# Optimization experiments

Measured on AMD Instinct MI355X. Metric: run time of the kernel, lower is better.

The kernel has to match this reference:

```python
import jax, jax.numpy as jnp
import numpy as np

N, E, G = 50000, 800000, 512
DIN, HID, DOUT, L, DE = 64, 64, 128, 3, 16
NEG_SLOPE = 0.2
BN_EPS = 1e-5


def setup_inputs() -> dict:
    key = jax.random.key(0)
    ks = jax.random.split(key, 20)
    s = 0.1  # weight scale for numerical stability
    return {
        "x": jax.random.normal(ks[0], (N, DIN), jnp.float32),
        "edge_index": jax.random.randint(ks[1], (2, E), 0, N, jnp.int32),
        "edge_attr": jax.random.normal(ks[2], (E, DE), jnp.float32),
        "batch": jnp.sort(jax.random.randint(ks[3], (N,), 0, G, jnp.int32)),
        "emb_W": jax.random.normal(ks[4], (HID, DIN), jnp.float32) * s,
        "emb_b": jax.random.normal(ks[5], (HID,), jnp.float32) * s,
        "Wl": jax.random.normal(ks[6], (L, HID, HID), jnp.float32) * s,
        "bl": jax.random.normal(ks[7], (L, HID), jnp.float32) * s,
        "Wr": jax.random.normal(ks[8], (L, HID, HID), jnp.float32) * s,
        "br": jax.random.normal(ks[9], (L, HID), jnp.float32) * s,
        "We": jax.random.normal(ks[10], (L, HID, DE), jnp.float32) * s,
        "att": jax.random.normal(ks[11], (L, HID), jnp.float32) * s,
        "conv_bias": jax.random.normal(ks[12], (L, HID), jnp.float32) * s,
        "bn_gamma": jax.random.uniform(ks[13], (L, HID), jnp.float32, 0.5, 1.5),
        "bn_beta": jax.random.normal(ks[14], (L, HID), jnp.float32) * s,
        "bn_mean": jnp.zeros((L, HID), jnp.float32),
        "bn_var": jnp.ones((L, HID), jnp.float32),
        "lin_W": jax.random.normal(ks[15], (DOUT, HID), jnp.float32) * s,
        "lin_b": jax.random.normal(ks[16], (DOUT,), jnp.float32) * s,
    }


def _gatv2(h, src, dst, edge_attr, Wl, bl, Wr, br, We, att, bias):
    # GATv2Conv, heads=1, concat=False, with edge features
    xl = h @ Wl.T + bl                      # [N,C] source transform (also message value)
    xr = h @ Wr.T + br                      # [N,C] target transform
    ea = edge_attr @ We.T                   # [E,C]
    m = xl[src] + xr[dst] + ea              # [E,C]
    m = jax.nn.leaky_relu(m, NEG_SLOPE)
    alpha = m @ att                         # [E] attention logits
    amax = jax.ops.segment_max(alpha, dst, num_segments=N)
    ea_exp = jnp.exp(alpha - amax[dst])
    denom = jax.ops.segment_sum(ea_exp, dst, num_segments=N)
    alpha = ea_exp / (denom[dst] + 1e-16)
    out = jax.ops.segment_sum(alpha[:, None] * xl[src], dst, num_segments=N)
    return out + bias


def reference(x, edge_index, edge_attr, batch, emb_W, emb_b, Wl, bl, Wr, br,
              We, att, conv_bias, bn_gamma, bn_beta, bn_mean, bn_var, lin_W, lin_b):
    src, dst = edge_index[0], edge_index[1]
    h = x @ emb_W.T + emb_b
    for i in range(L):
        hc = _gatv2(h, src, dst, edge_attr, Wl[i], bl[i], Wr[i], br[i],
                    We[i], att[i], conv_bias[i])
        # BatchNorm (eval mode, running stats)
        hc = (hc - bn_mean[i]) * jax.lax.rsqrt(bn_var[i] + BN_EPS) * bn_gamma[i] + bn_beta[i]
        hc = jax.nn.gelu(hc, approximate=False)  # torch F.gelu default is exact erf
        h = h + hc                                # residual; dropout p=0 / eval -> identity
    out = h @ lin_W.T + lin_b                     # [N,DOUT]
    counts = jax.ops.segment_sum(jnp.ones((N,), out.dtype), batch, num_segments=G)
    pooled = jax.ops.segment_sum(out, batch, num_segments=G)
    return pooled / jnp.maximum(counts, 1.0)[:, None]
```

## Files before the change

kernel.cpp:

```cpp
#include <hip/hip_runtime.h>
#include <math.h>

#define NEG_SLOPE 0.2f
#define BN_EPS 1e-5f

template <int N> struct IC { static constexpr int v = N; };
template <bool B> struct BC { static constexpr bool v = B; };

typedef _Float16 half2v __attribute__((ext_vector_type(2)));

__device__ __forceinline__ half2v u2h(unsigned u) {
  union { unsigned u; half2v h; } c;
  c.u = u;
  return c.h;
}
__device__ __forceinline__ unsigned pkh(float lo, float hi) {
  union { half2v h; unsigned u; } c;
  c.h[0] = (_Float16)lo;
  c.h[1] = (_Float16)hi;
  return c.u;
}

#if defined(__has_builtin)
#if __has_builtin(__builtin_amdgcn_fdot2)
#define FDOT2(a, b, c) __builtin_amdgcn_fdot2((a), (b), (c), false)
#endif
#endif
#ifndef FDOT2
__device__ __forceinline__ float fdot2_sw(half2v a, half2v b, float c) {
  return c + (float)a[0] * (float)b[0] + (float)a[1] * (float)b[1];
}
#define FDOT2(a, b, c) fdot2_sw((a), (b), (c))
#endif

#if defined(__has_builtin)
#if __has_builtin(__builtin_amdgcn_exp2f)
#define FEXP(x) __builtin_amdgcn_exp2f(x)
#define ATT_SCALE 1.44269504088896f
#endif
#endif
#ifndef FEXP
#define FEXP(x) __expf(x)
#define ATT_SCALE 1.0f
#endif

#define FMA4(acc, v, wq) \
  acc += (v).x * (wq).x + (v).y * (wq).y + (v).z * (wq).z + (v).w * (wq).w

#define DOT_ROW(buf, r, bias, OUT)                                     \
  {                                                                    \
    __builtin_amdgcn_sched_barrier(0);                                 \
    float a0 = 0.f, a1 = 0.f, a2 = 0.f, a3 = 0.f;                      \
    _Pragma("unroll") for (int q = 0; q < 4; q++) {                    \
      float4 v0 = *(const float4*)((buf) + (r) * 64 + q * 16 + 0);     \
      float4 v1 = *(const float4*)((buf) + (r) * 64 + q * 16 + 4);     \
      float4 v2 = *(const float4*)((buf) + (r) * 64 + q * 16 + 8);     \
      float4 v3 = *(const float4*)((buf) + (r) * 64 + q * 16 + 12);    \
      FMA4(a0, v0, W[q * 4 + 0]);                                      \
      FMA4(a1, v1, W[q * 4 + 1]);                                      \
      FMA4(a2, v2, W[q * 4 + 2]);                                      \
      FMA4(a3, v3, W[q * 4 + 3]);                                      \
    }                                                                  \
    OUT = (bias) + ((a0 + a1) + (a2 + a3));                            \
  }

__device__ __forceinline__ float wave_sum64(float v) {
  int x;
  x = __builtin_amdgcn_update_dpp(0, __float_as_int(v), 0x121, 0xF, 0xF, true);
  v += __int_as_float(x);
  x = __builtin_amdgcn_update_dpp(0, __float_as_int(v), 0x122, 0xF, 0xF, true);
  v += __int_as_float(x);
  x = __builtin_amdgcn_update_dpp(0, __float_as_int(v), 0x124, 0xF, 0xF, true);
  v += __int_as_float(x);
  x = __builtin_amdgcn_update_dpp(0, __float_as_int(v), 0x128, 0xF, 0xF, true);
  v += __int_as_float(x);
  x = __builtin_amdgcn_update_dpp(0, __float_as_int(v), 0x142, 0xF, 0xF, true);
  v += __int_as_float(x);
  x = __builtin_amdgcn_update_dpp(0, __float_as_int(v), 0x143, 0xF, 0xF, true);
  v += __int_as_float(x);
  return __int_as_float(__builtin_amdgcn_readlane(__float_as_int(v), 63));
}

__global__ __launch_bounds__(256) void hist_kernel(
    const int* __restrict__ dst, const int* __restrict__ batch,
    int* __restrict__ deg, float* __restrict__ counts, int E_, int N_) {
  int i = blockIdx.x * 256 + threadIdx.x;
  if (i < E_) atomicAdd(&deg[dst[i]], 1);
  if (i < N_) atomicAdd(&counts[batch[i]], 1.0f);
}

__global__ __launch_bounds__(256) void scanA_kernel(
    const int* __restrict__ deg, int* __restrict__ row_ptr,
    int* __restrict__ segTot, int N_, int nseg) {
  __shared__ int sb[256];
  int t = threadIdx.x;
  for (int s = blockIdx.x; s < nseg; s += gridDim.x) {
    int i = s * 256 + t;
    int v = (i < N_) ? deg[i] : 0;
    sb[t] = v;
    __syncthreads();
    for (int off = 1; off < 256; off <<= 1) {
      int a = (t >= off) ? sb[t - off] : 0;
      __syncthreads();
      sb[t] += a;
      __syncthreads();
    }
    int incl = sb[t];
    if (i < N_) row_ptr[i] = incl - v;
    if (t == 255) segTot[s] = incl;
    __syncthreads();
  }
}

__global__ __launch_bounds__(256) void scanB_kernel(int* __restrict__ segTot,
                                                    int nseg) {
  __shared__ int sb[256];
  __shared__ int baseSh;
  int t = threadIdx.x;
  if (t == 0) baseSh = 0;
  __syncthreads();
  for (int c0 = 0; c0 < nseg; c0 += 256) {
    int s = c0 + t;
    int v = (s < nseg) ? segTot[s] : 0;
    sb[t] = v;
    __syncthreads();
    for (int off = 1; off < 256; off <<= 1) {
      int a = (t >= off) ? sb[t - off] : 0;
      __syncthreads();
      sb[t] += a;
      __syncthreads();
    }
    int incl = sb[t];
    int base = baseSh;
    if (s < nseg) segTot[s] = base + incl - v;
    __syncthreads();
    if (t == 255) baseSh = base + incl;
    __syncthreads();
  }
}

__global__ __launch_bounds__(256) void scanC_kernel(
    int* __restrict__ row_ptr, const int* __restrict__ segTot,
    int* __restrict__ cursor, int N_, int E_) {
  int tid = blockIdx.x * 256 + threadIdx.x;
  int nt = gridDim.x * 256;
  for (int i = tid; i < N_; i += nt) {
    int rp = row_ptr[i] + segTot[i >> 8];
    row_ptr[i] = rp;
    cursor[i] = rp;
  }
  if (tid == 0) row_ptr[N_] = E_;
}

__global__ __launch_bounds__(256) void scatter_kernel(
    const int* __restrict__ src, const int* __restrict__ dst,
    int* __restrict__ cursor, int* __restrict__ csr_src,
    int* __restrict__ csr_eid, int E_) {
  int e = blockIdx.x * 256 + threadIdx.x;
  if (e >= E_) return;
  int pos = atomicAdd(&cursor[dst[e]], 1);
  csr_src[pos] = src[e];
  csr_eid[pos] = e;
}

__global__ __launch_bounds__(256) void permute_attr_kernel(
    const float4* __restrict__ edge_attr4, const int* __restrict__ csr_eid,
    unsigned* __restrict__ attr_u, int E_) {
  int p = blockIdx.x * 256 + threadIdx.x;
  if (p >= E_) return;
  int e = csr_eid[p];
  float4 a0 = edge_attr4[(size_t)e * 4 + 0];
  float4 a1 = edge_attr4[(size_t)e * 4 + 1];
  float4 a2 = edge_attr4[(size_t)e * 4 + 2];
  float4 a3 = edge_attr4[(size_t)e * 4 + 3];
  uint4 u0, u1;
  u0.x = pkh(a0.x, a0.y);
  u0.y = pkh(a0.z, a0.w);
  u0.z = pkh(a1.x, a1.y);
  u0.w = pkh(a1.z, a1.w);
  u1.x = pkh(a2.x, a2.y);
  u1.y = pkh(a2.z, a2.w);
  u1.z = pkh(a3.x, a3.y);
  u1.w = pkh(a3.z, a3.w);
  uint4* d4 = (uint4*)(attr_u + (size_t)p * 8);
  d4[0] = u0;
  d4[1] = u1;
}

__global__ __launch_bounds__(256, 3) void emb_lin0_kernel(
    const float* __restrict__ x, const float* __restrict__ emb_W,
    const float* __restrict__ emb_b, const float* __restrict__ Wl0,
    const float* __restrict__ bl0, const float* __restrict__ Wr0,
    const float* __restrict__ br0, float* __restrict__ h,
    _Float16* __restrict__ xl, _Float16* __restrict__ xr, int rows) {
  __shared__ float sx[4096];
  __shared__ float sh[4096];
  int lane = threadIdx.x & 63;
  int w = threadIdx.x >> 6;
  int n0 = blockIdx.x * 64;

  {
    int gmax = rows * 64 - 4;
#pragma unroll
    for (int i = 0; i < 4; i++) {
      int off = w * 1024 + i * 256 + lane * 4;
      int g = min(n0 * 64 + off, gmax);
      *(float4*)(sx + off) = *(const float4*)(x + g);
    }
  }

  float4 W[16];
  float b;

#pragma unroll
  for (int q = 0; q < 16; q++) W[q] = ((const float4*)(emb_W + lane * 64))[q];
  b = emb_b[lane];
#pragma unroll 1
  for (int t = 0; t < 16; t++) {
    int r = w * 16 + t;
    float a;
    DOT_ROW(sx, r, b, a);
    sh[r * 64 + lane] = a;
    int n = n0 + r;
    if (n < rows) h[(size_t)n * 64 + lane] = a;
  }

#pragma unroll
  for (int q = 0; q < 16; q++) W[q] = ((const float4*)(Wl0 + lane * 64))[q];
  b = bl0[lane];
#pragma unroll 1
  for (int t = 0; t < 16; t++) {
    int r = w * 16 + t;
    float a;
    DOT_ROW(sh, r, b, a);
    int n = n0 + r;
    if (n < rows) xl[(size_t)n * 64 + lane] = (_Float16)a;
  }

#pragma unroll
  for (int q = 0; q < 16; q++) W[q] = ((const float4*)(Wr0 + lane * 64))[q];
  b = br0[lane];
#pragma unroll 1
  for (int t = 0; t < 16; t++) {
    int r = w * 16 + t;
    float a;
    DOT_ROW(sh, r, b, a);
    int n = n0 + r;
    if (n < rows) xr[(size_t)n * 64 + lane] = (_Float16)a;
  }
}

__global__ __launch_bounds__(256, 3) void linx2_kernel(
    const float* __restrict__ in, const float* __restrict__ Wl,
    const float* __restrict__ bl, const float* __restrict__ Wr,
    const float* __restrict__ br, _Float16* __restrict__ xl,
    _Float16* __restrict__ xr, int rows) {
  __shared__ float sx[4096];
  int lane = threadIdx.x & 63;
  int w = threadIdx.x >> 6;
  int n0 = blockIdx.x * 64;

  {
    int gmax = rows * 64 - 4;
#pragma unroll
    for (int i = 0; i < 4; i++) {
      int off = w * 1024 + i * 256 + lane * 4;
      int g = min(n0 * 64 + off, gmax);
      *(float4*)(sx + off) = *(const float4*)(in + g);
    }
  }

  float4 W[16];
  float b;

#pragma unroll
  for (int q = 0; q < 16; q++) W[q] = ((const float4*)(Wl + lane * 64))[q];
  b = bl[lane];
#pragma unroll 1
  for (int t = 0; t < 16; t++) {
    int r = w * 16 + t;
    float a;
    DOT_ROW(sx, r, b, a);
    int n = n0 + r;
    if (n < rows) xl[(size_t)n * 64 + lane] = (_Float16)a;
  }

#pragma unroll
  for (int q = 0; q < 16; q++) W[q] = ((const float4*)(Wr + lane * 64))[q];
  b = br[lane];
#pragma unroll 1
  for (int t = 0; t < 16; t++) {
    int r = w * 16 + t;
    float a;
    DOT_ROW(sx, r, b, a);
    int n = n0 + r;
    if (n < rows) xr[(size_t)n * 64 + lane] = (_Float16)a;
  }
}

template <bool CONTIG>
__global__ __launch_bounds__(256) void gat_fused_kernel(
    const int* __restrict__ csr_src, const int* __restrict__ csr_eid,
    const int* __restrict__ row_ptr, const unsigned* __restrict__ attr_u,
    const float* __restrict__ edge_attr, const _Float16* __restrict__ xl,
    const _Float16* __restrict__ xr, const float* __restrict__ We,
    const float* __restrict__ att, const float* __restrict__ conv_bias,
    const float* __restrict__ gamma, const float* __restrict__ beta,
    const float* __restrict__ mean, const float* __restrict__ var,
    float* __restrict__ h, int N_) {
  int d = (blockIdx.x * 256 + threadIdx.x) >> 6;
  if (d >= N_) return;
  int j = threadIdx.x & 63;
  half2v Wek2[8];
  float Wekf[16];
  if constexpr (CONTIG) {
#pragma unroll
    for (int q = 0; q < 8; q++) {
      Wek2[q][0] = (_Float16)We[j * 16 + 2 * q];
      Wek2[q][1] = (_Float16)We[j * 16 + 2 * q + 1];
    }
  } else {
#pragma unroll
    for (int k = 0; k < 16; k++) Wekf[k] = We[j * 16 + k];
  }
  float att_j = att[j] * ATT_SCALE;
  float sc = rsqrtf(var[j] + BN_EPS) * gamma[j];
  float sh = (conv_bias[j] - mean[j]) * sc + beta[j];

  int beg = __builtin_amdgcn_readfirstlane(row_ptr[d]);
  int end = __builtin_amdgcn_readfirstlane(row_ptr[d + 1]);
  float xrj = (float)xr[(size_t)d * 64 + j];
  float m = -INFINITY, l = 0.f, acc = 0.f;

  auto chunk = [&](int base, auto C_, auto PAD_) {
    constexpr int C = decltype(C_)::v;
    constexpr bool PAD = decltype(PAD_)::v;
    int si[C];
#pragma unroll
    for (int t = 0; t < C; t++) {
      int idx = PAD ? min(base + t, end - 1) : (base + t);
      si[t] = csr_src[idx];
    }
    float xlv[C];
#pragma unroll
    for (int t = 0; t < C; t++)
      xlv[t] = (float)xl[(size_t)si[t] * 64 + j];
    float v[C];
#pragma unroll
    for (int t = 0; t < C; t++) {
      int idx = PAD ? min(base + t, end - 1) : (base + t);
      float ea;
      if constexpr (CONTIG) {
        const uint4* ap = (const uint4*)(attr_u + (size_t)idx * 8);
        uint4 ua = ap[0], ub = ap[1];
        ea = 0.f;
        ea = FDOT2(u2h(ua.x), Wek2[0], ea);
        ea = FDOT2(u2h(ua.y), Wek2[1], ea);
        ea = FDOT2(u2h(ua.z), Wek2[2], ea);
        ea = FDOT2(u2h(ua.w), Wek2[3], ea);
        ea = FDOT2(u2h(ub.x), Wek2[4], ea);
        ea = FDOT2(u2h(ub.y), Wek2[5], ea);
        ea = FDOT2(u2h(ub.z), Wek2[6], ea);
        ea = FDOT2(u2h(ub.w), Wek2[7], ea);
      } else {
        const float4* ap =
            (const float4*)(edge_attr + (size_t)csr_eid[idx] * 16);
        float4 a0 = ap[0], a1 = ap[1], a2 = ap[2], a3 = ap[3];
        ea = a0.x * Wekf[0]  + a0.y * Wekf[1]  + a0.z * Wekf[2]  + a0.w * Wekf[3]
           + a1.x * Wekf[4]  + a1.y * Wekf[5]  + a1.z * Wekf[6]  + a1.w * Wekf[7]
           + a2.x * Wekf[8]  + a2.y * Wekf[9]  + a2.z * Wekf[10] + a2.w * Wekf[11]
           + a3.x * Wekf[12] + a3.y * Wekf[13] + a3.z * Wekf[14] + a3.w * Wekf[15];
      }
      float z = xlv[t] + xrj + ea;
      z = fmaxf(z, NEG_SLOPE * z);
      float p = wave_sum64(z * att_j);
      v[t] = (!PAD || (base + t < end)) ? p : -INFINITY;
    }
    float mc = v[0];
#pragma unroll
    for (int t = 1; t < C; t++) mc = fmaxf(mc, v[t]);
    float newm = fmaxf(m, mc);
    float s = FEXP(m - newm);
    l *= s;
    acc *= s;
#pragma unroll
    for (int t = 0; t < C; t++) {
      float w = FEXP(v[t] - newm);
      l += w;
      acc += w * xlv[t];
    }
    m = newm;
  };

  int base = beg;
  for (; base + 16 <= end; base += 16) chunk(base, IC<16>{}, BC<false>{});
  if (base + 8 <= end) {
    chunk(base, IC<8>{}, BC<false>{});
    base += 8;
  }
  if (base < end) chunk(base, IC<8>{}, BC<true>{});

  float val = acc / (l + 1e-16f) * sc + sh;
  float g = 0.5f * val * (1.f + erff(val * 0.70710678118654752f));
  h[(size_t)d * 64 + j] += g;
}

__global__ __launch_bounds__(256, 2) void lin_pool_kernel(
    const float* __restrict__ h, const float* __restrict__ lin_W,
    const float* __restrict__ lin_b, const int* __restrict__ batch,
    const float* __restrict__ counts, float* __restrict__ pooled, int rows) {
  __shared__ float shh[4096];
  int lane = threadIdx.x & 63;
  int w = threadIdx.x >> 6;
  int n0 = blockIdx.x * 64;

  {
    int gmax = rows * 64 - 4;
#pragma unroll
    for (int i = 0; i < 4; i++) {
      int off = w * 1024 + i * 256 + lane * 4;
      int g = min(n0 * 64 + off, gmax);
      *(float4*)(shh + off) = *(const float4*)(h + g);
    }
  }

  float4 W0[16], W1[16];
#pragma unroll
  for (int q = 0; q < 16; q++) W0[q] = ((const float4*)(lin_W + lane * 64))[q];
#pragma unroll
  for (int q = 0; q < 16; q++)
    W1[q] = ((const float4*)(lin_W + (lane + 64) * 64))[q];
  float b0 = lin_b[lane], b1 = lin_b[lane + 64];

  int curg = -1;
  float acc0 = 0.f, acc1 = 0.f;
  int lim = min(16, rows - n0 - w * 16);
#pragma unroll 1
  for (int t = 0; t < lim; t++) {
    int r = w * 16 + t;
    __builtin_amdgcn_sched_barrier(0);
    float d0 = b0, d1 = b1;
#pragma unroll
    for (int q = 0; q < 16; q++) {
      float4 v = *(const float4*)(shh + r * 64 + q * 4);
      FMA4(d0, v, W0[q]);
      FMA4(d1, v, W1[q]);
    }
    int g = batch[n0 + r];
    if (g != curg) {
      if (curg >= 0) {
        float inv = 1.f / fmaxf(counts[curg], 1.f);
        atomicAdd(&pooled[curg * 128 + lane], acc0 * inv);
        atomicAdd(&pooled[curg * 128 + 64 + lane], acc1 * inv);
      }
      curg = g;
      acc0 = 0.f;
      acc1 = 0.f;
    }
    acc0 += d0;
    acc1 += d1;
  }
  if (curg >= 0) {
    float inv = 1.f / fmaxf(counts[curg], 1.f);
    atomicAdd(&pooled[curg * 128 + lane], acc0 * inv);
    atomicAdd(&pooled[curg * 128 + 64 + lane], acc1 * inv);
  }
}

extern "C" void kernel_launch(void* const* d_in, const int* in_sizes, int n_in,
                              void* d_out, int out_size, void* d_ws, size_t ws_size,
                              hipStream_t stream) {
  const float* x         = (const float*)d_in[0];
  const int*   edge_index= (const int*)  d_in[1];
  const float* edge_attr = (const float*)d_in[2];
  const int*   batch     = (const int*)  d_in[3];
  const float* emb_W     = (const float*)d_in[4];
  const float* emb_b     = (const float*)d_in[5];
  const float* Wl        = (const float*)d_in[6];
  const float* bl        = (const float*)d_in[7];
  const float* Wr        = (const float*)d_in[8];
  const float* br        = (const float*)d_in[9];
  const float* We        = (const float*)d_in[10];
  const float* att       = (const float*)d_in[11];
  const float* conv_bias = (const float*)d_in[12];
  const float* bn_gamma  = (const float*)d_in[13];
  const float* bn_beta   = (const float*)d_in[14];
  const float* bn_mean   = (const float*)d_in[15];
  const float* bn_var    = (const float*)d_in[16];
  const float* lin_W     = (const float*)d_in[17];
  const float* lin_b     = (const float*)d_in[18];

  const int N_ = in_sizes[0] / 64;
  const int E_ = in_sizes[1] / 2;
  const int G_ = out_size / 128;
  const int* src = edge_index;
  const int* dst = edge_index + E_;

  const int Npad = (N_ + 3) & ~3;
  const int Epad = (E_ + 19) & ~3;
  const int nseg = (N_ + 255) / 256;

  float* ws      = (float*)d_ws;
  float* h       = ws;
  _Float16* xl   = (_Float16*)(h + (size_t)N_ * 64);
  _Float16* xr   = xl + (size_t)N_ * 64;
  int*   csr_src = (int*)(xr + (size_t)N_ * 64);
  int*   csr_eid = csr_src + Epad;
  int*   row_ptr = csr_eid + Epad;
  int*   cursor  = row_ptr + (Npad + 4);
  int*   deg     = cursor + Npad;
  float* counts  = (float*)(deg + Npad);
  int*   segTot  = (int*)(counts + G_);
  uintptr_t abp  = (uintptr_t)(segTot + nseg + 8);
  abp = (abp + 15) & ~(uintptr_t)15;
  unsigned* attr_u = (unsigned*)abp;

  size_t base_bytes = (abp - (uintptr_t)d_ws);
  bool contig = ws_size >= base_bytes + (size_t)E_ * 32 + 64;

  const int hgrid = (max(E_, N_) + 255) / 256;
  const int ngrid = (N_ + 255) / 256;
  const int egrid = (E_ + 255) / 256;

  hipMemsetAsync(deg, 0, ((size_t)Npad + G_) * 4, stream);
  hist_kernel<<<hgrid, 256, 0, stream>>>(dst, batch, deg, counts, E_, N_);
  scanA_kernel<<<min(nseg, 1024), 256, 0, stream>>>(deg, row_ptr, segTot, N_,
                                                    nseg);
  scanB_kernel<<<1, 256, 0, stream>>>(segTot, nseg);
  scanC_kernel<<<ngrid, 256, 0, stream>>>(row_ptr, segTot, cursor, N_, E_);
  scatter_kernel<<<egrid, 256, 0, stream>>>(src, dst, cursor, csr_src,
                                            csr_eid, E_);
  if (contig) {
    permute_attr_kernel<<<egrid, 256, 0, stream>>>(
        (const float4*)edge_attr, csr_eid, attr_u, E_);
  }

  const int tgrid = (N_ + 63) / 64;
  emb_lin0_kernel<<<tgrid, 256, 0, stream>>>(x, emb_W, emb_b, Wl, bl, Wr, br,
                                             h, xl, xr, N_);

  const int gatBlocks = (N_ + 3) / 4;
  for (int l = 0; l < 3; l++) {
    if (l > 0) {
      linx2_kernel<<<tgrid, 256, 0, stream>>>(
          h, Wl + (size_t)l * 4096, bl + l * 64, Wr + (size_t)l * 4096,
          br + l * 64, xl, xr, N_);
    }
    if (contig) {
      gat_fused_kernel<true><<<gatBlocks, 256, 0, stream>>>(
          csr_src, csr_eid, row_ptr, attr_u, edge_attr, xl, xr,
          We + (size_t)l * 1024, att + l * 64, conv_bias + l * 64,
          bn_gamma + l * 64, bn_beta + l * 64, bn_mean + l * 64,
          bn_var + l * 64, h, N_);
    } else {
      gat_fused_kernel<false><<<gatBlocks, 256, 0, stream>>>(
          csr_src, csr_eid, row_ptr, attr_u, edge_attr, xl, xr,
          We + (size_t)l * 1024, att + l * 64, conv_bias + l * 64,
          bn_gamma + l * 64, bn_beta + l * 64, bn_mean + l * 64,
          bn_var + l * 64, h, N_);
    }
  }

  hipMemsetAsync(d_out, 0, (size_t)G_ * 128 * 4, stream);
  lin_pool_kernel<<<(N_ + 63) / 64, 256, 0, stream>>>(
      h, lin_W, lin_b, batch, counts, (float*)d_out, N_);
}
```

Baseline: 627.7 us.

## Map one node row per thread with weights read as uniform loads

```diff
diff --git a/kernel.cpp b/kernel.cpp
--- a/kernel.cpp
+++ b/kernel.cpp
@@ -47,21 +47,21 @@
 #define FMA4(acc, v, wq) \
   acc += (v).x * (wq).x + (v).y * (wq).y + (v).z * (wq).z + (v).w * (wq).w
 
-#define DOT_ROW(buf, r, bias, OUT)                                     \
-  {                                                                    \
-    __builtin_amdgcn_sched_barrier(0);                                 \
-    float a0 = 0.f, a1 = 0.f, a2 = 0.f, a3 = 0.f;                      \
-    _Pragma("unroll") for (int q = 0; q < 4; q++) {                    \
-      float4 v0 = *(const float4*)((buf) + (r) * 64 + q * 16 + 0);     \
-      float4 v1 = *(const float4*)((buf) + (r) * 64 + q * 16 + 4);     \
-      float4 v2 = *(const float4*)((buf) + (r) * 64 + q * 16 + 8);     \
-      float4 v3 = *(const float4*)((buf) + (r) * 64 + q * 16 + 12);    \
-      FMA4(a0, v0, W[q * 4 + 0]);                                      \
-      FMA4(a1, v1, W[q * 4 + 1]);                                      \
-      FMA4(a2, v2, W[q * 4 + 2]);                                      \
-      FMA4(a3, v3, W[q * 4 + 3]);                                      \
-    }                                                                  \
-    OUT = (bias) + ((a0 + a1) + (a2 + a3));                            \
+#define WDOT(Wp, bias, OUT)                                   \
+  {                                                           \
+    __builtin_amdgcn_sched_barrier(0);                        \
+    float a0 = 0.f, a1 = 0.f, a2 = 0.f, a3 = 0.f;             \
+    _Pragma("unroll") for (int k = 0; k < 4; k++) {           \
+      float4 w0 = ((const float4*)(Wp))[k * 4 + 0];           \
+      float4 w1 = ((const float4*)(Wp))[k * 4 + 1];           \
+      float4 w2 = ((const float4*)(Wp))[k * 4 + 2];           \
+      float4 w3 = ((const float4*)(Wp))[k * 4 + 3];           \
+      FMA4(a0, R[k * 4 + 0], w0);                             \
+      FMA4(a1, R[k * 4 + 1], w1);                             \
+      FMA4(a2, R[k * 4 + 2], w2);                             \
+      FMA4(a3, R[k * 4 + 3], w3);                             \
+    }                                                         \
+    OUT = (bias) + ((a0 + a1) + (a2 + a3));                   \
   }
 
 __device__ __forceinline__ float wave_sum64(float v) {
@@ -187,114 +187,77 @@
   d4[1] = u1;
 }
 
-__global__ __launch_bounds__(256, 3) void emb_lin0_kernel(
+__global__ __launch_bounds__(64) void emb_kernel(
     const float* __restrict__ x, const float* __restrict__ emb_W,
-    const float* __restrict__ emb_b, const float* __restrict__ Wl0,
-    const float* __restrict__ bl0, const float* __restrict__ Wr0,
-    const float* __restrict__ br0, float* __restrict__ h,
-    _Float16* __restrict__ xl, _Float16* __restrict__ xr, int rows) {
-  __shared__ float sx[4096];
-  __shared__ float sh[4096];
+    const float* __restrict__ emb_b, float* __restrict__ h, int rows) {
   int lane = threadIdx.x & 63;
-  int w = threadIdx.x >> 6;
-  int n0 = blockIdx.x * 64;
-
+  int n = blockIdx.x * 64 + lane;
+  int nc = min(n, rows - 1);
+  float4 R[16];
   {
-    int gmax = rows * 64 - 4;
-#pragma unroll
-    for (int i = 0; i < 4; i++) {
-      int off = w * 1024 + i * 256 + lane * 4;
-      int g = min(n0 * 64 + off, gmax);
-      *(float4*)(sx + off) = *(const float4*)(x + g);
-    }
-  }
-
-  float4 W[16];
-  float b;
-
-#pragma unroll
-  for (int q = 0; q < 16; q++) W[q] = ((const float4*)(emb_W + lane * 64))[q];
-  b = emb_b[lane];
+    const float4* xp = (const float4*)(x + (size_t)nc * 64);
+#pragma unroll
+    for (int q = 0; q < 16; q++) R[q] = xp[q];
+  }
+  bool ok = (n < rows);
+  float4* hp = (float4*)(h + (size_t)nc * 64);
 #pragma unroll 1
-  for (int t = 0; t < 16; t++) {
-    int r = w * 16 + t;
-    float a;
-    DOT_ROW(sx, r, b, a);
-    sh[r * 64 + lane] = a;
-    int n = n0 + r;
-    if (n < rows) h[(size_t)n * 64 + lane] = a;
-  }
-
-#pragma unroll
-  for (int q = 0; q < 16; q++) W[q] = ((const float4*)(Wl0 + lane * 64))[q];
-  b = bl0[lane];
-#pragma unroll 1
-  for (int t = 0; t < 16; t++) {
-    int r = w * 16 + t;
-    float a;
-    DOT_ROW(sh, r, b, a);
-    int n = n0 + r;
-    if (n < rows) xl[(size_t)n * 64 + lane] = (_Float16)a;
-  }
-
-#pragma unroll
-  for (int q = 0; q < 16; q++) W[q] = ((const float4*)(Wr0 + lane * 64))[q];
-  b = br0[lane];
-#pragma unroll 1
-  for (int t = 0; t < 16; t++) {
-    int r = w * 16 + t;
-    float a;
-    DOT_ROW(sh, r, b, a);
-    int n = n0 + r;
-    if (n < rows) xr[(size_t)n * 64 + lane] = (_Float16)a;
-  }
-}
-
-__global__ __launch_bounds__(256, 3) void linx2_kernel(
+  for (int o4 = 0; o4 < 16; o4++) {
+    float4 out;
+    WDOT(emb_W + (o4 * 4 + 0) * 64, emb_b[o4 * 4 + 0], out.x);
+    WDOT(emb_W + (o4 * 4 + 1) * 64, emb_b[o4 * 4 + 1], out.y);
+    WDOT(emb_W + (o4 * 4 + 2) * 64, emb_b[o4 * 4 + 2], out.z);
+    WDOT(emb_W + (o4 * 4 + 3) * 64, emb_b[o4 * 4 + 3], out.w);
+    if (ok) hp[o4] = out;
+  }
+}
+
+__global__ __launch_bounds__(64) void linx_kernel(
     const float* __restrict__ in, const float* __restrict__ Wl,
     const float* __restrict__ bl, const float* __restrict__ Wr,
     const float* __restrict__ br, _Float16* __restrict__ xl,
     _Float16* __restrict__ xr, int rows) {
-  __shared__ float sx[4096];
   int lane = threadIdx.x & 63;
-  int w = threadIdx.x >> 6;
-  int n0 = blockIdx.x * 64;
-
+  int n = blockIdx.x * 64 + lane;
+  int nc = min(n, rows - 1);
+  float4 R[16];
   {
-    int gmax = rows * 64 - 4;
-#pragma unroll
-    for (int i = 0; i < 4; i++) {
-      int off = w * 1024 + i * 256 + lane * 4;
-      int g = min(n0 * 64 + off, gmax);
-      *(float4*)(sx + off) = *(const float4*)(in + g);
-    }
-  }
-
-  float4 W[16];
-  float b;
-
-#pragma unroll
-  for (int q = 0; q < 16; q++) W[q] = ((const float4*)(Wl + lane * 64))[q];
-  b = bl[lane];
+    const float4* xp = (const float4*)(in + (size_t)nc * 64);
+#pragma unroll
+    for (int q = 0; q < 16; q++) R[q] = xp[q];
+  }
+  bool ok = (n < rows);
+
+  uint2* xlp = (uint2*)(xl + (size_t)nc * 64);
 #pragma unroll 1
-  for (int t = 0; t < 16; t++) {
-    int r = w * 16 + t;
-    float a;
-    DOT_ROW(sx, r, b, a);
-    int n = n0 + r;
-    if (n < rows) xl[(size_t)n * 64 + lane] = (_Float16)a;
-  }
-
-#pragma unroll
-  for (int q = 0; q < 16; q++) W[q] = ((const float4*)(Wr + lane * 64))[q];
-  b = br[lane];
+  for (int o4 = 0; o4 < 16; o4++) {
+    float o0, o1, o2, o3;
+    WDOT(Wl + (o4 * 4 + 0) * 64, bl[o4 * 4 + 0], o0);
+    WDOT(Wl + (o4 * 4 + 1) * 64, bl[o4 * 4 + 1], o1);
+    WDOT(Wl + (o4 * 4 + 2) * 64, bl[o4 * 4 + 2], o2);
+    WDOT(Wl + (o4 * 4 + 3) * 64, bl[o4 * 4 + 3], o3);
+    if (ok) {
+      uint2 pk;
+      pk.x = pkh(o0, o1);
+      pk.y = pkh(o2, o3);
+      xlp[o4] = pk;
+    }
+  }
+
+  uint2* xrp = (uint2*)(xr + (size_t)nc * 64);
 #pragma unroll 1
-  for (int t = 0; t < 16; t++) {
-    int r = w * 16 + t;
-    float a;
-    DOT_ROW(sx, r, b, a);
-    int n = n0 + r;
-    if (n < rows) xr[(size_t)n * 64 + lane] = (_Float16)a;
+  for (int o4 = 0; o4 < 16; o4++) {
+    float o0, o1, o2, o3;
+    WDOT(Wr + (o4 * 4 + 0) * 64, br[o4 * 4 + 0], o0);
+    WDOT(Wr + (o4 * 4 + 1) * 64, br[o4 * 4 + 1], o1);
+    WDOT(Wr + (o4 * 4 + 2) * 64, br[o4 * 4 + 2], o2);
+    WDOT(Wr + (o4 * 4 + 3) * 64, br[o4 * 4 + 3], o3);
+    if (ok) {
+      uint2 pk;
+      pk.x = pkh(o0, o1);
+      pk.y = pkh(o2, o3);
+      xrp[o4] = pk;
+    }
   }
 }
 
@@ -535,14 +498,14 @@
         (const float4*)edge_attr, csr_eid, attr_u, E_);
   }
 
-  const int tgrid = (N_ + 63) / 64;
-  emb_lin0_kernel<<<tgrid, 256, 0, stream>>>(x, emb_W, emb_b, Wl, bl, Wr, br,
-                                             h, xl, xr, N_);
+  const int nblk64 = (N_ + 63) / 64;
+  emb_kernel<<<nblk64, 64, 0, stream>>>(x, emb_W, emb_b, h, N_);
+  linx_kernel<<<nblk64, 64, 0, stream>>>(h, Wl, bl, Wr, br, xl, xr, N_);
 
   const int gatBlocks = (N_ + 3) / 4;
   for (int l = 0; l < 3; l++) {
     if (l > 0) {
-      linx2_kernel<<<tgrid, 256, 0, stream>>>(
+      linx_kernel<<<nblk64, 64, 0, stream>>>(
           h, Wl + (size_t)l * 4096, bl + l * 64, Wr + (size_t)l * 4096,
           br + l * 64, xl, xr, N_);
     }
```

Result: slower. 863.9 us (+37.6%).

## Compute per-layer Wl/Wr node transforms with fp16 MFMA instead of scalar dots

Applied to the files above, without the earlier changes.

```diff
diff --git a/kernel.cpp b/kernel.cpp
--- a/kernel.cpp
+++ b/kernel.cpp
@@ -8,6 +8,8 @@
 template <bool B> struct BC { static constexpr bool v = B; };
 
 typedef _Float16 half2v __attribute__((ext_vector_type(2)));
+typedef _Float16 f16x8 __attribute__((ext_vector_type(8)));
+typedef float f32x4v __attribute__((ext_vector_type(4)));
 
 __device__ __forceinline__ half2v u2h(unsigned u) {
   union { unsigned u; half2v h; } c;
@@ -187,14 +189,21 @@
   d4[1] = u1;
 }
 
-__global__ __launch_bounds__(256, 3) void emb_lin0_kernel(
+__global__ __launch_bounds__(256) void pack_w16_kernel(
+    const float* __restrict__ Wl, const float* __restrict__ Wr,
+    _Float16* __restrict__ w16, int per) {
+  int i = blockIdx.x * 256 + threadIdx.x;
+  if (i < per) {
+    w16[i] = (_Float16)Wl[i];
+  } else if (i < 2 * per) {
+    w16[i] = (_Float16)Wr[i - per];
+  }
+}
+
+__global__ __launch_bounds__(256, 3) void emb_kernel(
     const float* __restrict__ x, const float* __restrict__ emb_W,
-    const float* __restrict__ emb_b, const float* __restrict__ Wl0,
-    const float* __restrict__ bl0, const float* __restrict__ Wr0,
-    const float* __restrict__ br0, float* __restrict__ h,
-    _Float16* __restrict__ xl, _Float16* __restrict__ xr, int rows) {
+    const float* __restrict__ emb_b, float* __restrict__ h, int rows) {
   __shared__ float sx[4096];
-  __shared__ float sh[4096];
   int lane = threadIdx.x & 63;
   int w = threadIdx.x >> 6;
   int n0 = blockIdx.x * 64;
@@ -210,92 +219,88 @@
   }
 
   float4 W[16];
-  float b;
-
 #pragma unroll
   for (int q = 0; q < 16; q++) W[q] = ((const float4*)(emb_W + lane * 64))[q];
-  b = emb_b[lane];
-#pragma unroll 1
-  for (int t = 0; t < 16; t++) {
-    int r = w * 16 + t;
-    float a;
-    DOT_ROW(sx, r, b, a);
-    sh[r * 64 + lane] = a;
-    int n = n0 + r;
-    if (n < rows) h[(size_t)n * 64 + lane] = a;
-  }
-
-#pragma unroll
-  for (int q = 0; q < 16; q++) W[q] = ((const float4*)(Wl0 + lane * 64))[q];
-  b = bl0[lane];
-#pragma unroll 1
-  for (int t = 0; t < 16; t++) {
-    int r = w * 16 + t;
-    float a;
-    DOT_ROW(sh, r, b, a);
-    int n = n0 + r;
-    if (n < rows) xl[(size_t)n * 64 + lane] = (_Float16)a;
-  }
-
-#pragma unroll
-  for (int q = 0; q < 16; q++) W[q] = ((const float4*)(Wr0 + lane * 64))[q];
-  b = br0[lane];
-#pragma unroll 1
-  for (int t = 0; t < 16; t++) {
-    int r = w * 16 + t;
-    float a;
-    DOT_ROW(sh, r, b, a);
-    int n = n0 + r;
-    if (n < rows) xr[(size_t)n * 64 + lane] = (_Float16)a;
-  }
-}
-
-__global__ __launch_bounds__(256, 3) void linx2_kernel(
-    const float* __restrict__ in, const float* __restrict__ Wl,
-    const float* __restrict__ bl, const float* __restrict__ Wr,
-    const float* __restrict__ br, _Float16* __restrict__ xl,
-    _Float16* __restrict__ xr, int rows) {
-  __shared__ float sx[4096];
-  int lane = threadIdx.x & 63;
-  int w = threadIdx.x >> 6;
-  int n0 = blockIdx.x * 64;
-
-  {
-    int gmax = rows * 64 - 4;
-#pragma unroll
-    for (int i = 0; i < 4; i++) {
-      int off = w * 1024 + i * 256 + lane * 4;
-      int g = min(n0 * 64 + off, gmax);
-      *(float4*)(sx + off) = *(const float4*)(in + g);
-    }
-  }
-
-  float4 W[16];
-  float b;
-
-#pragma unroll
-  for (int q = 0; q < 16; q++) W[q] = ((const float4*)(Wl + lane * 64))[q];
-  b = bl[lane];
+  float b = emb_b[lane];
 #pragma unroll 1
   for (int t = 0; t < 16; t++) {
     int r = w * 16 + t;
     float a;
     DOT_ROW(sx, r, b, a);
     int n = n0 + r;
-    if (n < rows) xl[(size_t)n * 64 + lane] = (_Float16)a;
-  }
-
-#pragma unroll
-  for (int q = 0; q < 16; q++) W[q] = ((const float4*)(Wr + lane * 64))[q];
-  b = br[lane];
-#pragma unroll 1
-  for (int t = 0; t < 16; t++) {
-    int r = w * 16 + t;
-    float a;
-    DOT_ROW(sx, r, b, a);
-    int n = n0 + r;
-    if (n < rows) xr[(size_t)n * 64 + lane] = (_Float16)a;
-  }
+    if (n < rows) h[(size_t)n * 64 + lane] = a;
+  }
+}
+
+#if defined(__has_builtin)
+#if __has_builtin(__builtin_amdgcn_mfma_f32_16x16x32_f16)
+#define HAVE_MFMA16 1
+#endif
+#endif
+
+__global__ __launch_bounds__(256) void linx_mfma_kernel(
+    const float* __restrict__ in, const _Float16* __restrict__ Wl16,
+    const float* __restrict__ bl, const _Float16* __restrict__ Wr16,
+    const float* __restrict__ br, _Float16* __restrict__ xl,
+    _Float16* __restrict__ xr, int rows) {
+#ifdef HAVE_MFMA16
+  int lane = threadIdx.x & 63;
+  int w = threadIdx.x >> 6;
+  int n0 = blockIdx.x * 64 + w * 16;
+  int r = lane & 15;
+  int kg = lane >> 4;
+
+  int nA = min(n0 + r, rows - 1);
+  f16x8 A0, A1;
+  {
+    const float* p = in + (size_t)nA * 64 + kg * 8;
+    float4 xa = *(const float4*)(p);
+    float4 xb = *(const float4*)(p + 4);
+    A0[0] = (_Float16)xa.x; A0[1] = (_Float16)xa.y;
+    A0[2] = (_Float16)xa.z; A0[3] = (_Float16)xa.w;
+    A0[4] = (_Float16)xb.x; A0[5] = (_Float16)xb.y;
+    A0[6] = (_Float16)xb.z; A0[7] = (_Float16)xb.w;
+    xa = *(const float4*)(p + 32);
+    xb = *(const float4*)(p + 36);
+    A1[0] = (_Float16)xa.x; A1[1] = (_Float16)xa.y;
+    A1[2] = (_Float16)xa.z; A1[3] = (_Float16)xa.w;
+    A1[4] = (_Float16)xb.x; A1[5] = (_Float16)xb.y;
+    A1[6] = (_Float16)xb.z; A1[7] = (_Float16)xb.w;
+  }
+
+#pragma unroll
+  for (int c = 0; c < 4; c++) {
+    int o = c * 16 + r;
+    {
+      const f16x8* b0 = (const f16x8*)(Wl16 + (size_t)o * 64 + kg * 8);
+      const f16x8* b1 = (const f16x8*)(Wl16 + (size_t)o * 64 + 32 + kg * 8);
+      f32x4v acc;
+      float bv = bl[o];
+      acc[0] = bv; acc[1] = bv; acc[2] = bv; acc[3] = bv;
+      acc = __builtin_amdgcn_mfma_f32_16x16x32_f16(A0, b0[0], acc, 0, 0, 0);
+      acc = __builtin_amdgcn_mfma_f32_16x16x32_f16(A1, b1[0], acc, 0, 0, 0);
+#pragma unroll
+      for (int g = 0; g < 4; g++) {
+        int nd = n0 + kg * 4 + g;
+        if (nd < rows) xl[(size_t)nd * 64 + o] = (_Float16)acc[g];
+      }
+    }
+    {
+      const f16x8* b0 = (const f16x8*)(Wr16 + (size_t)o * 64 + kg * 8);
+      const f16x8* b1 = (const f16x8*)(Wr16 + (size_t)o * 64 + 32 + kg * 8);
+      f32x4v acc;
+      float bv = br[o];
+      acc[0] = bv; acc[1] = bv; acc[2] = bv; acc[3] = bv;
+      acc = __builtin_amdgcn_mfma_f32_16x16x32_f16(A0, b0[0], acc, 0, 0, 0);
+      acc = __builtin_amdgcn_mfma_f32_16x16x32_f16(A1, b1[0], acc, 0, 0, 0);
+#pragma unroll
+      for (int g = 0; g < 4; g++) {
+        int nd = n0 + kg * 4 + g;
+        if (nd < rows) xr[(size_t)nd * 64 + o] = (_Float16)acc[g];
+      }
+    }
+  }
+#endif
 }
 
 template <bool CONTIG>
@@ -513,9 +518,11 @@
   int*   segTot  = (int*)(counts + G_);
   uintptr_t abp  = (uintptr_t)(segTot + nseg + 8);
   abp = (abp + 15) & ~(uintptr_t)15;
-  unsigned* attr_u = (unsigned*)abp;
-
-  size_t base_bytes = (abp - (uintptr_t)d_ws);
+  _Float16* w16  = (_Float16*)abp;
+  uintptr_t abp2 = abp + 24576 * sizeof(_Float16);
+  unsigned* attr_u = (unsigned*)abp2;
+
+  size_t base_bytes = (abp2 - (uintptr_t)d_ws);
   bool contig = ws_size >= base_bytes + (size_t)E_ * 32 + 64;
 
   const int hgrid = (max(E_, N_) + 255) / 256;
@@ -535,17 +542,16 @@
         (const float4*)edge_attr, csr_eid, attr_u, E_);
   }
 
+  pack_w16_kernel<<<(24576 + 255) / 256, 256, 0, stream>>>(Wl, Wr, w16,
+                                                           12288);
   const int tgrid = (N_ + 63) / 64;
-  emb_lin0_kernel<<<tgrid, 256, 0, stream>>>(x, emb_W, emb_b, Wl, bl, Wr, br,
-                                             h, xl, xr, N_);
+  emb_kernel<<<tgrid, 256, 0, stream>>>(x, emb_W, emb_b, h, N_);
 
   const int gatBlocks = (N_ + 3) / 4;
   for (int l = 0; l < 3; l++) {
-    if (l > 0) {
-      linx2_kernel<<<tgrid, 256, 0, stream>>>(
-          h, Wl + (size_t)l * 4096, bl + l * 64, Wr + (size_t)l * 4096,
-          br + l * 64, xl, xr, N_);
-    }
+    linx_mfma_kernel<<<tgrid, 256, 0, stream>>>(
+        h, w16 + (size_t)l * 4096, bl + l * 64, w16 + 12288 + (size_t)l * 4096,
+        br + l * 64, xl, xr, N_);
     if (contig) {
       gat_fused_kernel<true><<<gatBlocks, 256, 0, stream>>>(
           csr_src, csr_eid, row_ptr, attr_u, edge_attr, xl, xr,
```

Result: faster. 564.9 us (-10.0%).
